# Optimization experiments

Measured on AMD Instinct MI355X. Metric: run time of the kernel, lower is better.

The kernel has to match this reference:

```python
import jax, jax.numpy as jnp
import numpy as np

NUM_USERS = 1024
NUM_BUSINESSES = 2048
N_NODES = NUM_USERS + NUM_BUSINESSES  # 3072
B = 1024            # batch size (== NUM_USERS to keep the business_idx-offset bug valid)
E = 16384           # edges (self loops added inside reference, PyG GATConv default)
H = 768             # hidden_size
HEADS = 8
NUM_IMAGES = 3


def setup_inputs() -> dict:
    key = jax.random.key(0)
    ks = jax.random.split(key, 24)
    def rn(k, shape, s=0.02):
        return jax.random.normal(k, shape, dtype=jnp.float32) * s
    inp = {
        'text_cls': rn(ks[0], (B, 768), 1.0),              # BERT CLS features
        'img_cls': rn(ks[1], (B, NUM_IMAGES, 768), 1.0),   # ViT CLS features per image
        'biz_feats': rn(ks[2], (B, 3), 1.0),
        'W_text': rn(ks[3], (768, H)), 'b_text': jnp.zeros((H,), jnp.float32),
        'W_img': rn(ks[4], (768, H)), 'b_img': jnp.zeros((H,), jnp.float32),
        'W_bf': rn(ks[5], (3, H)), 'b_bf': jnp.zeros((H,), jnp.float32),
        'user_table': rn(ks[6], (NUM_USERS, H)),
        'biz_table': rn(ks[7], (NUM_BUSINESSES, H)),
        'W1': rn(ks[8], (H, HEADS * H)),
        'att_src1': rn(ks[9], (HEADS, H), 0.1),
        'att_dst1': rn(ks[10], (HEADS, H), 0.1),
        'b1': jnp.zeros((HEADS * H,), jnp.float32),
        'W2': rn(ks[11], (HEADS * H, H)),
        'att_src2': rn(ks[12], (1, H), 0.1),
        'att_dst2': rn(ks[13], (1, H), 0.1),
        'b2': jnp.zeros((H,), jnp.float32),
        'Wf1': rn(ks[14], (4 * H, 2 * H)), 'bf1': jnp.zeros((2 * H,), jnp.float32),
        'Wf2': rn(ks[15], (2 * H, H)), 'bf2': jnp.zeros((H,), jnp.float32),
        'Wf3': rn(ks[16], (H, 1)), 'bf3': jnp.zeros((1,), jnp.float32),
        'user_idx': jax.random.randint(ks[17], (B,), 0, NUM_USERS),
        'business_idx': jax.random.randint(ks[18], (B,), NUM_USERS, N_NODES),
        'edge_index': jax.random.randint(ks[19], (2, E), 0, N_NODES),
    }
    return inp


def gat_conv(x, src, dst, W, a_src, a_dst, bias, heads):
    # PyG GATConv: linear -> per-head additive attention -> scatter softmax over dst -> scatter add
    N = x.shape[0]
    C = W.shape[1] // heads
    h = (x @ W).reshape(N, heads, C)                       # [N,H,C]
    s_src = jnp.sum(h * a_src, axis=-1)                    # [N,H]
    s_dst = jnp.sum(h * a_dst, axis=-1)                    # [N,H]
    e = jax.nn.leaky_relu(s_src[src] + s_dst[dst], 0.2)    # [E,H]
    e_max = jax.ops.segment_max(e, dst, num_segments=N)    # [N,H]
    ee = jnp.exp(e - e_max[dst])
    denom = jax.ops.segment_sum(ee, dst, num_segments=N)   # [N,H]
    alpha = ee / (denom[dst] + 1e-16)                      # [E,H]
    out = jax.ops.segment_sum(h[src] * alpha[..., None], dst, num_segments=N)  # [N,H,C]
    return out.reshape(N, heads * C) + bias


def reference(text_cls, img_cls, biz_feats, W_text, b_text, W_img, b_img, W_bf, b_bf,
              user_table, biz_table, W1, att_src1, att_dst1, b1, W2, att_src2, att_dst2, b2,
              Wf1, bf1, Wf2, bf2, Wf3, bf3, user_idx, business_idx, edge_index):
    text_emb = text_cls @ W_text + b_text                       # TextEncoder.fc
    img_emb = jnp.mean(img_cls, axis=1) @ W_img + b_img         # ImageEncoder mean + fc
    meta = biz_feats @ W_bf + b_bf                              # business_feature_fc
    user_emb = user_table[user_idx]
    biz_emb = biz_table[business_idx - user_idx.shape[0]]       # faithful: offset by batch size
    x = jnp.zeros((N_NODES, H), jnp.float32)
    x = x.at[user_idx].set(user_emb)
    x = x.at[business_idx].set((text_emb + img_emb + meta + biz_emb) / 4.0)
    loop = jnp.arange(N_NODES)
    src = jnp.concatenate([edge_index[0], loop])                # add self loops (PyG default)
    dst = jnp.concatenate([edge_index[1], loop])
    x = jax.nn.relu(gat_conv(x, src, dst, W1, att_src1, att_dst1, b1, HEADS))
    x = gat_conv(x, src, dst, W2, att_src2, att_dst2, b2, 1)
    cat = jnp.concatenate([x[user_idx], x[business_idx], text_emb, img_emb], axis=1)  # [B,4H]
    h1 = jax.nn.relu(cat @ Wf1 + bf1)
    h2 = jax.nn.relu(h1 @ Wf2 + bf2)
    return (h2 @ Wf3 + bf3).squeeze(-1)                         # [B]
```

## Files before the change

kernel.cpp:

```cpp
#include <hip/hip_runtime.h>
#include <hip/hip_bf16.h>

namespace {

constexpr int kB = 1024;
constexpr int kNU = 1024;
constexpr int kNB = 2048;
constexpr int kNN = 3072;
constexpr int kE = 16384;
constexpr int kET = kE + kNN;
constexpr int kH = 768;
constexpr int kHeads = 8;
constexpr int kS2 = 8;

typedef __attribute__((ext_vector_type(8))) short bf16x8_t;
typedef __attribute__((ext_vector_type(4))) float f32x4_t;

__device__ __forceinline__ float tof(float x) { return x; }
__device__ __forceinline__ float tof(__hip_bfloat16 x) { return __bfloat162float(x); }
__device__ __forceinline__ void stor(float* p, float v) { *p = v; }
__device__ __forceinline__ void stor(__hip_bfloat16* p, float v) { *p = __float2bfloat16(v); }

__device__ __forceinline__ float blo(unsigned u) {
  union { unsigned u; float f; } c; c.u = u << 16; return c.f;
}
__device__ __forceinline__ float bhi(unsigned u) {
  union { unsigned u; float f; } c; c.u = u & 0xffff0000u; return c.f;
}

__device__ __forceinline__ unsigned pk2(float a, float b) {
  union { __hip_bfloat16 h[2]; unsigned u; } c;
  c.h[0] = __float2bfloat16(a); c.h[1] = __float2bfloat16(b);
  return c.u;
}

__device__ __forceinline__ void gload_lds16(const void* g, void* l) {
  __builtin_amdgcn_global_load_lds(
      (const __attribute__((address_space(1))) void*)g,
      (__attribute__((address_space(3))) void*)l, 16, 0, 0);
}

template <int BM, int BN, int FM, int FN, typename TC>
__device__ __forceinline__ void gemm_body(
    const __hip_bfloat16* __restrict__ A, const __hip_bfloat16* __restrict__ Bt,
    const float* __restrict__ bias, TC* __restrict__ C,
    int K, int lda, int ldc, int act, int bx, int by) {
  __shared__ __align__(16) __hip_bfloat16 As[2][BM][32];
  __shared__ __align__(16) __hip_bfloat16 Bs[2][BN][32];
  const int t = threadIdx.x;
  const int w = t >> 6, lane = t & 63;
  const int wm = w >> 1, wn = w & 1;
  const int bm = by * BM, bn = bx * BN;
  const int lr = lane & 15, lg = lane >> 4;

  f32x4_t acc[FM][FN];
#pragma unroll
  for (int m = 0; m < FM; ++m)
#pragma unroll
    for (int n = 0; n < FN; ++n) acc[m][n] = (f32x4_t){0.f, 0.f, 0.f, 0.f};

  auto stage = [&](int buf, int kt) {
    const int k0 = kt << 5;
#pragma unroll
    for (int i = 0; i < BM / 64; ++i) {
      int L = i * 256 + t;
      gload_lds16(A + (size_t)(bm + (L >> 2)) * lda + k0 + (L & 3) * 8,
                  (char*)(&As[buf][0][0]) + ((size_t)(i * 256 + w * 64)) * 16);
    }
#pragma unroll
    for (int i = 0; i < BN / 64; ++i) {
      int L = i * 256 + t;
      gload_lds16(Bt + (size_t)(bn + (L >> 2)) * K + k0 + (L & 3) * 8,
                  (char*)(&Bs[buf][0][0]) + ((size_t)(i * 256 + w * 64)) * 16);
    }
  };

  const int NT = K >> 5;
  stage(0, 0);
  __syncthreads();
  for (int kt = 0; kt < NT; ++kt) {
    const int cur = kt & 1;
    if (kt + 1 < NT) stage(cur ^ 1, kt + 1);
    bf16x8_t af[FM], bv[FN];
#pragma unroll
    for (int m = 0; m < FM; ++m)
      af[m] = *(const bf16x8_t*)&As[cur][wm * FM * 16 + m * 16 + lr][lg * 8];
#pragma unroll
    for (int n = 0; n < FN; ++n)
      bv[n] = *(const bf16x8_t*)&Bs[cur][wn * FN * 16 + n * 16 + lr][lg * 8];
#pragma unroll
    for (int m = 0; m < FM; ++m)
#pragma unroll
      for (int n = 0; n < FN; ++n)
        acc[m][n] = __builtin_amdgcn_mfma_f32_16x16x32_bf16(af[m], bv[n], acc[m][n], 0, 0, 0);
    __syncthreads();
  }

#pragma unroll
  for (int m = 0; m < FM; ++m) {
    const int row0 = bm + wm * FM * 16 + m * 16 + lg * 4;
#pragma unroll
    for (int n = 0; n < FN; ++n) {
      const int cn = bn + wn * FN * 16 + n * 16 + lr;
      const float bvv = bias ? bias[cn] : 0.f;
#pragma unroll
      for (int r = 0; r < 4; ++r) {
        float v = acc[m][n][r] + bvv;
        if (act) v = fmaxf(v, 0.f);
        stor(&C[(size_t)(row0 + r) * ldc + cn], v);
      }
    }
  }
}

__device__ __forceinline__ void swz_xy(bool mfast, int& bx, int& by) {
  const int nwg = gridDim.x * gridDim.y;
  const int orig = blockIdx.y * gridDim.x + blockIdx.x;
  const int swz = (orig & 7) * (nwg >> 3) + (orig >> 3);
  if (mfast) { by = swz % gridDim.y; bx = swz / gridDim.y; }
  else       { bx = swz % gridDim.x; by = swz / gridDim.x; }
}

template <int BM, int BN, int FM, int FN>
__global__ __launch_bounds__(256) void mfma_gemm_dual(
    const __hip_bfloat16* __restrict__ A0, const __hip_bfloat16* __restrict__ Bt0,
    const float* __restrict__ bias0, float* __restrict__ C0,
    const __hip_bfloat16* __restrict__ A1, const __hip_bfloat16* __restrict__ Bt1,
    const float* __restrict__ bias1, float* __restrict__ C1,
    int N, int K) {
  int bx, by;
  swz_xy(true, bx, by);
  const __hip_bfloat16* A = blockIdx.z ? A1 : A0;
  const __hip_bfloat16* Bt = blockIdx.z ? Bt1 : Bt0;
  const float* bias = blockIdx.z ? bias1 : bias0;
  float* C = blockIdx.z ? C1 : C0;
  gemm_body<BM, BN, FM, FN, float>(A, Bt, bias, C, K, K, N, 0, bx, by);
}

template <int BM, int BN, int FM, int FN>
__global__ __launch_bounds__(256) void gemm_head(
    const __hip_bfloat16* __restrict__ y, const __hip_bfloat16* __restrict__ W1t,
    const float* __restrict__ b1, __hip_bfloat16* __restrict__ x2) {
  const int hd = blockIdx.x;
  const int tile = blockIdx.y;
  const int bx = tile % (kH / BN);
  const int by = tile / (kH / BN);
  gemm_body<BM, BN, FM, FN, __hip_bfloat16>(
      y + (size_t)hd * kH, W1t + (size_t)hd * kH * kH, b1 + hd * kH,
      x2 + (size_t)hd * kH, kH, kHeads * kH, kHeads * kH, 1, bx, by);
}

template <int BM, int BN, int FM, int FN, int S>
__global__ __launch_bounds__(256) void mfma_gemm_kpin(
    const __hip_bfloat16* __restrict__ A, const __hip_bfloat16* __restrict__ Bt,
    float* __restrict__ Cpart, int M, int N, int K) {
  __shared__ __align__(16) __hip_bfloat16 As[2][BM][32];
  __shared__ __align__(16) __hip_bfloat16 Bs[2][BN][32];
  const int kc = blockIdx.x;
  const int tile = blockIdx.y;
  const int tilesN = N / BN;
  const int bx = tile % tilesN;
  const int by = tile / tilesN;
  const int KC = K / S;
  const int kbeg = kc * KC;
  const int t = threadIdx.x;
  const int w = t >> 6, lane = t & 63;
  const int wm = w >> 1, wn = w & 1;
  const int bm = by * BM, bn = bx * BN;
  const int lr = lane & 15, lg = lane >> 4;

  f32x4_t acc[FM][FN];
#pragma unroll
  for (int m = 0; m < FM; ++m)
#pragma unroll
    for (int n = 0; n < FN; ++n) acc[m][n] = (f32x4_t){0.f, 0.f, 0.f, 0.f};

  auto stage = [&](int buf, int kt) {
    const int k0 = kbeg + (kt << 5);
#pragma unroll
    for (int i = 0; i < BM / 64; ++i) {
      int L = i * 256 + t;
      gload_lds16(A + (size_t)(bm + (L >> 2)) * K + k0 + (L & 3) * 8,
                  (char*)(&As[buf][0][0]) + ((size_t)(i * 256 + w * 64)) * 16);
    }
#pragma unroll
    for (int i = 0; i < BN / 64; ++i) {
      int L = i * 256 + t;
      gload_lds16(Bt + (size_t)(bn + (L >> 2)) * K + k0 + (L & 3) * 8,
                  (char*)(&Bs[buf][0][0]) + ((size_t)(i * 256 + w * 64)) * 16);
    }
  };

  const int NT = KC >> 5;
  stage(0, 0);
  __syncthreads();
  for (int kt = 0; kt < NT; ++kt) {
    const int cur = kt & 1;
    if (kt + 1 < NT) stage(cur ^ 1, kt + 1);
    bf16x8_t af[FM], bv[FN];
#pragma unroll
    for (int m = 0; m < FM; ++m)
      af[m] = *(const bf16x8_t*)&As[cur][wm * FM * 16 + m * 16 + lr][lg * 8];
#pragma unroll
    for (int n = 0; n < FN; ++n)
      bv[n] = *(const bf16x8_t*)&Bs[cur][wn * FN * 16 + n * 16 + lr][lg * 8];
#pragma unroll
    for (int m = 0; m < FM; ++m)
#pragma unroll
      for (int n = 0; n < FN; ++n)
        acc[m][n] = __builtin_amdgcn_mfma_f32_16x16x32_bf16(af[m], bv[n], acc[m][n], 0, 0, 0);
    __syncthreads();
  }

  float* Cp = Cpart + (size_t)kc * M * N;
#pragma unroll
  for (int m = 0; m < FM; ++m) {
    const int row0 = bm + wm * FM * 16 + m * 16 + lg * 4;
#pragma unroll
    for (int n = 0; n < FN; ++n) {
      const int cn = bn + wn * FN * 16 + n * 16 + lr;
#pragma unroll
      for (int r = 0; r < 4; ++r) Cp[(size_t)(row0 + r) * N + cn] = acc[m][n][r];
    }
  }
}

template <int BM, int BN, int FM, int FN>
__global__ __launch_bounds__(256) void mfma_gemm_splitk(
    const __hip_bfloat16* __restrict__ A, const __hip_bfloat16* __restrict__ Bt,
    float* __restrict__ Cpart, int M, int N, int K, int KC) {
  __shared__ __align__(16) __hip_bfloat16 As[2][BM][32];
  __shared__ __align__(16) __hip_bfloat16 Bs[2][BN][32];
  int bx, by;
  swz_xy(false, bx, by);
  const int t = threadIdx.x;
  const int w = t >> 6, lane = t & 63;
  const int wm = w >> 1, wn = w & 1;
  const int bm = by * BM, bn = bx * BN;
  const int kbeg = blockIdx.z * KC;
  const int lr = lane & 15, lg = lane >> 4;

  f32x4_t acc[FM][FN];
#pragma unroll
  for (int m = 0; m < FM; ++m)
#pragma unroll
    for (int n = 0; n < FN; ++n) acc[m][n] = (f32x4_t){0.f, 0.f, 0.f, 0.f};

  auto stage = [&](int buf, int kt) {
    const int k0 = kbeg + (kt << 5);
#pragma unroll
    for (int i = 0; i < BM / 64; ++i) {
      int L = i * 256 + t;
      gload_lds16(A + (size_t)(bm + (L >> 2)) * K + k0 + (L & 3) * 8,
                  (char*)(&As[buf][0][0]) + ((size_t)(i * 256 + w * 64)) * 16);
    }
#pragma unroll
    for (int i = 0; i < BN / 64; ++i) {
      int L = i * 256 + t;
      gload_lds16(Bt + (size_t)(bn + (L >> 2)) * K + k0 + (L & 3) * 8,
                  (char*)(&Bs[buf][0][0]) + ((size_t)(i * 256 + w * 64)) * 16);
    }
  };

  const int NT = KC >> 5;
  stage(0, 0);
  __syncthreads();
  for (int kt = 0; kt < NT; ++kt) {
    const int cur = kt & 1;
    if (kt + 1 < NT) stage(cur ^ 1, kt + 1);
    bf16x8_t af[FM], bv[FN];
#pragma unroll
    for (int m = 0; m < FM; ++m)
      af[m] = *(const bf16x8_t*)&As[cur][wm * FM * 16 + m * 16 + lr][lg * 8];
#pragma unroll
    for (int n = 0; n < FN; ++n)
      bv[n] = *(const bf16x8_t*)&Bs[cur][wn * FN * 16 + n * 16 + lr][lg * 8];
#pragma unroll
    for (int m = 0; m < FM; ++m)
#pragma unroll
      for (int n = 0; n < FN; ++n)
        acc[m][n] = __builtin_amdgcn_mfma_f32_16x16x32_bf16(af[m], bv[n], acc[m][n], 0, 0, 0);
    __syncthreads();
  }

  float* Cp = Cpart + (size_t)blockIdx.z * M * N;
#pragma unroll
  for (int m = 0; m < FM; ++m) {
    const int row0 = bm + wm * FM * 16 + m * 16 + lg * 4;
#pragma unroll
    for (int n = 0; n < FN; ++n) {
      const int cn = bn + wn * FN * 16 + n * 16 + lr;
#pragma unroll
      for (int r = 0; r < 4; ++r) Cp[(size_t)(row0 + r) * N + cn] = acc[m][n][r];
    }
  }
}

__global__ __launch_bounds__(192) void reduce_scores2_kernel(
    const float* __restrict__ part, const float* __restrict__ att_src,
    const float* __restrict__ att_dst, __hip_bfloat16* __restrict__ h2,
    float* __restrict__ s_src, float* __restrict__ s_dst) {
  __shared__ float redS[3], redD[3];
  const int row = blockIdx.x;
  const int t = threadIdx.x;
  const int c = t * 4;
  const float* p = part + (size_t)row * kH + c;
  float4 s = *(const float4*)p;
#pragma unroll
  for (int z = 1; z < kS2; ++z) {
    float4 qv = *(const float4*)(p + (size_t)z * kNN * kH);
    s.x += qv.x; s.y += qv.y; s.z += qv.z; s.w += qv.w;
  }
  __hip_bfloat16 b0 = __float2bfloat16(s.x), b1 = __float2bfloat16(s.y);
  __hip_bfloat16 b2 = __float2bfloat16(s.z), b3 = __float2bfloat16(s.w);
  __hip_bfloat16* o = h2 + (size_t)row * kH + c;
  o[0] = b0; o[1] = b1; o[2] = b2; o[3] = b3;
  float f0 = tof(b0), f1 = tof(b1), f2 = tof(b2), f3 = tof(b3);
  float ss = f0 * att_src[c] + f1 * att_src[c + 1] + f2 * att_src[c + 2] + f3 * att_src[c + 3];
  float sd = f0 * att_dst[c] + f1 * att_dst[c + 1] + f2 * att_dst[c + 2] + f3 * att_dst[c + 3];
#pragma unroll
  for (int off = 32; off; off >>= 1) { ss += __shfl_down(ss, off); sd += __shfl_down(sd, off); }
  if ((t & 63) == 0) { redS[t >> 6] = ss; redD[t >> 6] = sd; }
  __syncthreads();
  if (t == 0) {
    s_src[row] = redS[0] + redS[1] + redS[2];
    s_dst[row] = redD[0] + redD[1] + redD[2];
  }
}

__global__ void reduce_relu_kernel(const float* __restrict__ part,
                                   const float* __restrict__ bias,
                                   __hip_bfloat16* __restrict__ outb, int MN4, int N) {
  int i = blockIdx.x * 256 + threadIdx.x;
  if (i >= MN4) return;
  float4 s = ((const float4*)part)[i];
  float4 p = ((const float4*)part)[(size_t)MN4 + i];
  int c = (i * 4) % N;
  float v0 = fmaxf(s.x + p.x + bias[c], 0.f);
  float v1 = fmaxf(s.y + p.y + bias[c + 1], 0.f);
  float v2 = fmaxf(s.z + p.z + bias[c + 2], 0.f);
  float v3 = fmaxf(s.w + p.w + bias[c + 3], 0.f);
  uint2 o;
  o.x = pk2(v0, v1); o.y = pk2(v2, v3);
  *(uint2*)(outb + (size_t)i * 4) = o;
}

__global__ __launch_bounds__(192) void reduce_final_kernel(
    const float* __restrict__ part, const float* __restrict__ bias,
    const float* __restrict__ Wf3, const float* __restrict__ bf3,
    float* __restrict__ out) {
  __shared__ float red[3];
  const int row = blockIdx.x;
  const int t = threadIdx.x;
  const int c = t * 4;
  const float* p0 = part + (size_t)row * kH + c;
  const float* p1 = p0 + (size_t)kB * kH;
  float4 a = *(const float4*)p0;
  float4 b = *(const float4*)p1;
  float v0 = fmaxf(a.x + b.x + bias[c], 0.f);
  float v1 = fmaxf(a.y + b.y + bias[c + 1], 0.f);
  float v2 = fmaxf(a.z + b.z + bias[c + 2], 0.f);
  float v3 = fmaxf(a.w + b.w + bias[c + 3], 0.f);
  float s = v0 * Wf3[c] + v1 * Wf3[c + 1] + v2 * Wf3[c + 2] + v3 * Wf3[c + 3];
#pragma unroll
  for (int off = 32; off; off >>= 1) s += __shfl_down(s, off);
  if ((t & 63) == 0) red[t >> 6] = s;
  __syncthreads();
  if (t == 0) out[row] = red[0] + red[1] + red[2] + bf3[0];
}

struct TJobs {
  const float* in[6];
  __hip_bfloat16* out[6];
  int K[6];
  int N[6];
  int start[7];
};

__global__ __launch_bounds__(256) void transp_prep_kernel(
    TJobs j, const float* __restrict__ text_cls, const float* __restrict__ img_cls,
    __hip_bfloat16* __restrict__ text_bf, __hip_bfloat16* __restrict__ imgm_bf,
    int prep_blocks, const float* __restrict__ W1, const float* __restrict__ a_src,
    const float* __restrict__ a_dst, float* __restrict__ wa,
    int wa_blocks, uint4* __restrict__ xb4, int* __restrict__ deg,
    int* __restrict__ winner) {
  __shared__ float tl[32][33];
  const int bid = blockIdx.x;
  const int t = threadIdx.x;
  if (bid >= j.start[6] + prep_blocks + wa_blocks) {
    int i = (bid - j.start[6] - prep_blocks - wa_blocks) * 256 + t;
    if (i < kNN * kH * 2 / 16) xb4[i] = (uint4){0u, 0u, 0u, 0u};
    if (i < kNN) deg[i] = 0;
    if (i < kNB) winner[i] = -1;
    return;
  }
  if (bid >= j.start[6] + prep_blocks) {
    int gw = ((bid - j.start[6] - prep_blocks) * 256 + t) >> 6;
    int lane = t & 63;
    if (gw >= kHeads * kH) return;
    int i = gw >> 3, hd = gw & 7;
    const float* wrow = W1 + (size_t)i * (kHeads * kH) + hd * kH;
    const float* as = a_src + (size_t)hd * kH;
    const float* ad = a_dst + (size_t)hd * kH;
    float ss = 0.f, sd = 0.f;
    for (int c = lane; c < kH; c += 64) {
      float wv = wrow[c];
      ss = fmaf(wv, as[c], ss);
      sd = fmaf(wv, ad[c], sd);
    }
#pragma unroll
    for (int o = 32; o; o >>= 1) { ss += __shfl_down(ss, o); sd += __shfl_down(sd, o); }
    if (lane == 0) {
      wa[hd * kH + i] = ss;
      wa[kHeads * kH + hd * kH + i] = sd;
    }
    return;
  }
  if (bid >= j.start[6]) {
    int idx = (bid - j.start[6]) * 256 + t;
    if (idx < kB * kH) {
      text_bf[idx] = __float2bfloat16(text_cls[idx]);
      int b = idx / kH, c = idx - b * kH;
      const float* p = img_cls + (size_t)b * 3 * kH + c;
      imgm_bf[idx] = __float2bfloat16((p[0] + p[kH] + p[2 * kH]) * (1.f / 3.f));
    }
    return;
  }
  int idx = 0;
#pragma unroll
  for (int q = 1; q < 6; ++q)
    if (bid >= j.start[q]) idx = q;
  const int tile = bid - j.start[idx];
  const int N = j.N[idx], K = j.K[idx];
  const int tilesN = N >> 5;
  const int n0 = (tile % tilesN) << 5, k0 = (tile / tilesN) << 5;
  const float* in = j.in[idx];
  __hip_bfloat16* out = j.out[idx];
  const int r = t >> 3, c = (t & 7) * 4;
#pragma unroll
  for (int i = 0; i < 4; ++i) tl[r][c + i] = in[(size_t)(k0 + r) * N + n0 + c + i];
  __syncthreads();
  __hip_bfloat16* op = out + (size_t)(n0 + r) * K + k0 + c;
#pragma unroll
  for (int i = 0; i < 4; ++i) op[i] = __float2bfloat16(tl[c + i][r]);
}

__global__ __launch_bounds__(256) void s1_kernel(const __hip_bfloat16* __restrict__ xb,
                                                 const float* __restrict__ wa,
                                                 float* __restrict__ s1s,
                                                 float* __restrict__ s1d) {
  __shared__ unsigned xrow[kH / 2];
  const int n = blockIdx.x;
  const int t = threadIdx.x;
  const unsigned* xp = (const unsigned*)(xb + (size_t)n * kH);
  if (t < 128) { xrow[t] = xp[t]; xrow[t + 128] = xp[t + 128]; xrow[t + 256] = xp[t + 256]; }
  __syncthreads();
  const int w = t >> 6, lane = t & 63;
  const float* ws0 = wa + (size_t)w * kH;
  const float* wd0 = wa + (size_t)(kHeads + w) * kH;
  const float* ws1 = wa + (size_t)(w + 4) * kH;
  const float* wd1 = wa + (size_t)(kHeads + w + 4) * kH;
  float s0 = 0.f, d0 = 0.f, s1 = 0.f, d1 = 0.f;
  for (int u = lane; u < kH / 2; u += 64) {
    unsigned v = xrow[u];
    float f0 = blo(v), f1 = bhi(v);
    int c = u * 2;
    s0 = fmaf(f0, ws0[c], fmaf(f1, ws0[c + 1], s0));
    d0 = fmaf(f0, wd0[c], fmaf(f1, wd0[c + 1], d0));
    s1 = fmaf(f0, ws1[c], fmaf(f1, ws1[c + 1], s1));
    d1 = fmaf(f0, wd1[c], fmaf(f1, wd1[c + 1], d1));
  }
#pragma unroll
  for (int o = 32; o; o >>= 1) {
    s0 += __shfl_down(s0, o); d0 += __shfl_down(d0, o);
    s1 += __shfl_down(s1, o); d1 += __shfl_down(d1, o);
  }
  if (lane == 0) {
    s1s[n * 8 + w] = s0;     s1d[n * 8 + w] = d0;
    s1s[n * 8 + w + 4] = s1; s1d[n * 8 + w + 4] = d1;
  }
}

__global__ __launch_bounds__(256) void agg1x_kernel(
    const int* __restrict__ rowptr, const int* __restrict__ cols,
    const float* __restrict__ s1s, const float* __restrict__ s1d,
    const __hip_bfloat16* __restrict__ xb, __hip_bfloat16* __restrict__ y) {
  __shared__ float mh[8], rdh[8], sdl[8];
  __shared__ float alph[128][9];
  const int n = blockIdx.x;
  const int t = threadIdx.x, w = t >> 6, lane = t & 63;
  const int beg = rowptr[n], end = rowptr[n + 1];
  if (t < 8) sdl[t] = s1d[n * 8 + t];
  __syncthreads();
#pragma unroll
  for (int p = 0; p < 2; ++p) {
    const int h = w + p * 4;
    const float sd = sdl[h];
    float m = -3.402823466e38f;
    for (int i = beg + lane; i < end; i += 64) {
      float e = s1s[(size_t)cols[i] * 8 + h] + sd;
      e = (e > 0.f) ? e : 0.2f * e;
      m = fmaxf(m, e);
    }
#pragma unroll
    for (int o = 32; o; o >>= 1) m = fmaxf(m, __shfl_xor(m, o));
    float ds = 0.f;
    for (int i = beg + lane; i < end; i += 64) {
      float e = s1s[(size_t)cols[i] * 8 + h] + sd;
      e = (e > 0.f) ? e : 0.2f * e;
      ds += expf(e - m);
    }
#pragma unroll
    for (int o = 32; o; o >>= 1) ds += __shfl_xor(ds, o);
    if (lane == 0) { mh[h] = m; rdh[h] = 1.f / (ds + 1e-16f); }
  }
  __syncthreads();

  float acc[8][4];
#pragma unroll
  for (int h = 0; h < 8; ++h)
#pragma unroll
    for (int q = 0; q < 4; ++q) acc[h][q] = 0.f;
  const int c0 = t * 4;

  for (int chunk = beg; chunk < end; chunk += 128) {
    const int cnt = min(128, end - chunk);
#pragma unroll
    for (int p = 0; p < 2; ++p) {
      const int h = w + p * 4;
      const float sd = sdl[h], m = mh[h], rd = rdh[h];
      for (int i = lane; i < cnt; i += 64) {
        float e = s1s[(size_t)cols[chunk + i] * 8 + h] + sd;
        e = (e > 0.f) ? e : 0.2f * e;
        alph[i][h] = expf(e - m) * rd;
      }
    }
    __syncthreads();
    if (t < 192) {
      for (int i = 0; i < cnt; ++i) {
        int src = cols[chunk + i];
        uint2 v = *(const uint2*)(xb + (size_t)src * kH + c0);
        float f0 = blo(v.x), f1 = bhi(v.x), f2 = blo(v.y), f3 = bhi(v.y);
#pragma unroll
        for (int h = 0; h < 8; ++h) {
          float a = alph[i][h];
          acc[h][0] = fmaf(a, f0, acc[h][0]);
          acc[h][1] = fmaf(a, f1, acc[h][1]);
          acc[h][2] = fmaf(a, f2, acc[h][2]);
          acc[h][3] = fmaf(a, f3, acc[h][3]);
        }
      }
    }
    __syncthreads();
  }
  if (t < 192) {
#pragma unroll
    for (int h = 0; h < 8; ++h) {
      uint2 o;
      o.x = pk2(acc[h][0], acc[h][1]);
      o.y = pk2(acc[h][2], acc[h][3]);
      *(uint2*)(y + ((size_t)n * 8 + h) * kH + c0) = o;
    }
  }
}

__global__ void deg_winner_kernel(const int* __restrict__ ei, int* __restrict__ deg,
                                  const int* __restrict__ business_idx,
                                  int* __restrict__ winner) {
  int e = blockIdx.x * 256 + threadIdx.x;
  if (e < kET) {
    int dst = (e < kE) ? ei[kE + e] : (e - kE);
    atomicAdd(&deg[dst], 1);
  }
  if (e < kB) atomicMax(&winner[business_idx[e] - kNU], e);
}

__global__ __launch_bounds__(1024) void scan_kernel(const int* __restrict__ deg,
                                                    int* __restrict__ rowptr,
                                                    int* __restrict__ cursor) {
  __shared__ int sums[1024];
  int t = threadIdx.x;
  int v0 = deg[t * 3], v1 = deg[t * 3 + 1], v2 = deg[t * 3 + 2];
  int s = v0 + v1 + v2;
  sums[t] = s;
  __syncthreads();
  for (int o = 1; o < 1024; o <<= 1) {
    int xv = (t >= o) ? sums[t - o] : 0;
    __syncthreads();
    sums[t] += xv;
    __syncthreads();
  }
  int excl = sums[t] - s;
  rowptr[t * 3] = excl;          cursor[t * 3] = excl;
  rowptr[t * 3 + 1] = excl + v0; cursor[t * 3 + 1] = excl + v0;
  rowptr[t * 3 + 2] = excl + v0 + v1; cursor[t * 3 + 2] = excl + v0 + v1;
  if (t == 1023) rowptr[kNN] = excl + s;
}

__global__ void fill_kernel(const int* __restrict__ ei, int* __restrict__ cursor,
                            int* __restrict__ cols) {
  int e = blockIdx.x * 256 + threadIdx.x;
  if (e >= kET) return;
  int src, dst;
  if (e < kE) { src = ei[e]; dst = ei[kE + e]; } else { src = dst = e - kE; }
  int pos = atomicAdd(&cursor[dst], 1);
  cols[pos] = src;
}

__global__ void build_x_kernel(const int* __restrict__ user_idx,
                               const float* __restrict__ user_table,
                               const int* __restrict__ winner,
                               const float* __restrict__ text_emb,
                               const float* __restrict__ img_emb,
                               const float* __restrict__ biz_feats,
                               const float* __restrict__ W_bf,
                               const float* __restrict__ b_bf,
                               const float* __restrict__ biz_table,
                               __hip_bfloat16* __restrict__ xb) {
  int b = blockIdx.x;
  if (b < kNU) {
    int node = user_idx[b];
    for (int c = threadIdx.x; c < kH; c += blockDim.x)
      xb[(size_t)node * kH + c] = __float2bfloat16(user_table[(size_t)node * kH + c]);
  } else {
    int m = b - kNU;
    int w = winner[m];
    if (w < 0) return;
    int node = kNU + m;
    float f0 = biz_feats[w * 3], f1 = biz_feats[w * 3 + 1], f2 = biz_feats[w * 3 + 2];
    for (int c = threadIdx.x; c < kH; c += blockDim.x) {
      float meta = f0 * W_bf[c] + f1 * W_bf[kH + c] + f2 * W_bf[2 * kH + c] + b_bf[c];
      float v = (text_emb[(size_t)w * kH + c] + img_emb[(size_t)w * kH + c] + meta +
                 biz_table[(size_t)m * kH + c]) * 0.25f;
      xb[(size_t)node * kH + c] = __float2bfloat16(v);
    }
  }
}

__global__ __launch_bounds__(256) void gat_agg_kernel(
    const int* __restrict__ rowptr, const int* __restrict__ cols,
    const float* __restrict__ s_src, const float* __restrict__ s_dst,
    const __hip_bfloat16* __restrict__ h, const float* __restrict__ bias,
    float* __restrict__ out_f, int total) {
  const int pair = blockIdx.x * 4 + (threadIdx.x >> 6);
  if (pair >= total) return;
  const int lane = threadIdx.x & 63;
  const int n = pair;
  const int beg = rowptr[n], end = rowptr[n + 1];
  const float sdv = s_dst[pair];

  float m = -3.402823466e38f;
  for (int i = beg + lane; i < end; i += 64) {
    float e = s_src[cols[i]] + sdv;
    e = (e > 0.f) ? e : 0.2f * e;
    m = fmaxf(m, e);
  }
#pragma unroll
  for (int o = 32; o; o >>= 1) m = fmaxf(m, __shfl_xor(m, o));

  float dsum = 0.f;
  for (int i = beg + lane; i < end; i += 64) {
    float e = s_src[cols[i]] + sdv;
    e = (e > 0.f) ? e : 0.2f * e;
    dsum += expf(e - m);
  }
#pragma unroll
  for (int o = 32; o; o >>= 1) dsum += __shfl_xor(dsum, o);
  const float rdsum = 1.f / (dsum + 1e-16f);

  float a[12];
#pragma unroll
  for (int q = 0; q < 12; ++q) a[q] = 0.f;
  const size_t hoff = (size_t)lane * 4;
  for (int i = beg; i < end; ++i) {
    int src = cols[i];
    float e = s_src[src] + sdv;
    e = (e > 0.f) ? e : 0.2f * e;
    float wgt = expf(e - m) * rdsum;
    const __hip_bfloat16* hp = h + (size_t)src * kH + hoff;
#pragma unroll
    for (int j = 0; j < 3; ++j) {
      uint2 v = *(const uint2*)(hp + j * 256);
      a[j * 4 + 0] = fmaf(wgt, blo(v.x), a[j * 4 + 0]);
      a[j * 4 + 1] = fmaf(wgt, bhi(v.x), a[j * 4 + 1]);
      a[j * 4 + 2] = fmaf(wgt, blo(v.y), a[j * 4 + 2]);
      a[j * 4 + 3] = fmaf(wgt, bhi(v.y), a[j * 4 + 3]);
    }
  }
  const size_t ob = (size_t)n * kH + hoff;
#pragma unroll
  for (int j = 0; j < 3; ++j) {
#pragma unroll
    for (int q = 0; q < 4; ++q)
      out_f[ob + j * 256 + q] = a[j * 4 + q] + bias[hoff + j * 256 + q];
  }
}

__global__ void cat_kernel(const float* __restrict__ xf, const float* __restrict__ text_emb,
                           const float* __restrict__ img_emb, const int* __restrict__ user_idx,
                           const int* __restrict__ business_idx, __hip_bfloat16* __restrict__ cat) {
  int b = blockIdx.x;
  int u = user_idx[b], z = business_idx[b];
  __hip_bfloat16* crow = cat + (size_t)b * 4 * kH;
  for (int c = threadIdx.x; c < kH; c += blockDim.x) {
    crow[c] = __float2bfloat16(xf[(size_t)u * kH + c]);
    crow[kH + c] = __float2bfloat16(xf[(size_t)z * kH + c]);
    crow[2 * kH + c] = __float2bfloat16(text_emb[(size_t)b * kH + c]);
    crow[3 * kH + c] = __float2bfloat16(img_emb[(size_t)b * kH + c]);
  }
}

}

extern "C" void kernel_launch(void* const* d_in, const int* in_sizes, int n_in,
                              void* d_out, int out_size, void* d_ws, size_t ws_size,
                              hipStream_t stream) {
  const float* text_cls = (const float*)d_in[0];
  const float* img_cls = (const float*)d_in[1];
  const float* biz_feats = (const float*)d_in[2];
  const float* W_text = (const float*)d_in[3];
  const float* b_text = (const float*)d_in[4];
  const float* W_img = (const float*)d_in[5];
  const float* b_img = (const float*)d_in[6];
  const float* W_bf = (const float*)d_in[7];
  const float* b_bf = (const float*)d_in[8];
  const float* user_table = (const float*)d_in[9];
  const float* biz_table = (const float*)d_in[10];
  const float* W1 = (const float*)d_in[11];
  const float* att_src1 = (const float*)d_in[12];
  const float* att_dst1 = (const float*)d_in[13];
  const float* b1 = (const float*)d_in[14];
  const float* W2 = (const float*)d_in[15];
  const float* att_src2 = (const float*)d_in[16];
  const float* att_dst2 = (const float*)d_in[17];
  const float* b2 = (const float*)d_in[18];
  const float* Wf1 = (const float*)d_in[19];
  const float* bf1 = (const float*)d_in[20];
  const float* Wf2 = (const float*)d_in[21];
  const float* bf2 = (const float*)d_in[22];
  const float* Wf3 = (const float*)d_in[23];
  const float* bf3 = (const float*)d_in[24];
  const int* user_idx = (const int*)d_in[25];
  const int* business_idx = (const int*)d_in[26];
  const int* edge_index = (const int*)d_in[27];
  float* out = (float*)d_out;
  (void)in_sizes; (void)n_in; (void)out_size; (void)ws_size;

  char* base = (char*)d_ws;
  size_t off = 0;
  auto alloc = [&](size_t bytes) -> void* {
    void* p = base + off;
    off = (off + bytes + 255) & ~(size_t)255;
    return p;
  };
  __hip_bfloat16* xb = (__hip_bfloat16*)alloc((size_t)kNN * kH * 2);
  __hip_bfloat16* text_bf = (__hip_bfloat16*)alloc((size_t)kB * kH * 2);
  __hip_bfloat16* imgm_bf = (__hip_bfloat16*)alloc((size_t)kB * kH * 2);
  float* text_emb = (float*)alloc((size_t)kB * kH * 4);
  float* img_emb = (float*)alloc((size_t)kB * kH * 4);
  __hip_bfloat16* Wtt = (__hip_bfloat16*)alloc((size_t)kH * kH * 2);
  __hip_bfloat16* Wit = (__hip_bfloat16*)alloc((size_t)kH * kH * 2);
  __hip_bfloat16* W1t = (__hip_bfloat16*)alloc((size_t)kHeads * kH * kH * 2);
  __hip_bfloat16* W2t = (__hip_bfloat16*)alloc((size_t)kH * kHeads * kH * 2);
  __hip_bfloat16* Wf1t = (__hip_bfloat16*)alloc((size_t)2 * kH * 4 * kH * 2);
  __hip_bfloat16* Wf2t = (__hip_bfloat16*)alloc((size_t)kH * 2 * kH * 2);
  float* wa = (float*)alloc((size_t)2 * kHeads * kH * 4);
  __hip_bfloat16* y = (__hip_bfloat16*)alloc((size_t)kNN * kHeads * kH * 2);
  char* ext = (char*)alloc((size_t)kNN * kHeads * kH * 2);
  float* part = (float*)y;
  float* xf = (float*)ext;
  __hip_bfloat16* catb = (__hip_bfloat16*)(ext + 9437184);
  __hip_bfloat16* m1 = (__hip_bfloat16*)(ext + 9437184 + 6291456);
  __hip_bfloat16* x2 = (__hip_bfloat16*)alloc((size_t)kNN * kHeads * kH * 2);
  __hip_bfloat16* h2 = (__hip_bfloat16*)alloc((size_t)kNN * kH * 2);
  float* s1s = (float*)alloc((size_t)kNN * kHeads * 4);
  float* s1d = (float*)alloc((size_t)kNN * kHeads * 4);
  float* s2s = (float*)alloc((size_t)kNN * 4);
  float* s2d = (float*)alloc((size_t)kNN * 4);
  int* deg = (int*)alloc((size_t)kNN * 4);
  int* rowptr = (int*)alloc((size_t)(kNN + 1) * 4);
  int* cursor = (int*)alloc((size_t)kNN * 4);
  int* cols = (int*)alloc((size_t)kET * 4);
  int* winner = (int*)alloc((size_t)kNB * 4);

  TJobs tj;
  tj.in[0] = W_text; tj.out[0] = Wtt;  tj.K[0] = kH;          tj.N[0] = kH;
  tj.in[1] = W_img;  tj.out[1] = Wit;  tj.K[1] = kH;          tj.N[1] = kH;
  tj.in[2] = W1;     tj.out[2] = W1t;  tj.K[2] = kH;          tj.N[2] = kHeads * kH;
  tj.in[3] = W2;     tj.out[3] = W2t;  tj.K[3] = kHeads * kH; tj.N[3] = kH;
  tj.in[4] = Wf1;    tj.out[4] = Wf1t; tj.K[4] = 4 * kH;      tj.N[4] = 2 * kH;
  tj.in[5] = Wf2;    tj.out[5] = Wf2t; tj.K[5] = 2 * kH;      tj.N[5] = kH;
  tj.start[0] = 0;
  for (int q = 0; q < 6; ++q)
    tj.start[q + 1] = tj.start[q] + (tj.K[q] / 32) * (tj.N[q] / 32);
  const int prep_blocks = (kB * kH + 255) / 256;
  const int wa_blocks = (kHeads * kH) / 4;
  const int init_blocks = (kNN * kH * 2 / 16 + 255) / 256;
  transp_prep_kernel<<<tj.start[6] + prep_blocks + wa_blocks + init_blocks, 256, 0, stream>>>(
      tj, text_cls, img_cls, text_bf, imgm_bf, prep_blocks, W1, att_src1, att_dst1, wa,
      wa_blocks, (uint4*)xb, deg, winner);

  mfma_gemm_dual<64, 128, 2, 4><<<dim3(kH / 128, kB / 64, 2), 256, 0, stream>>>(
      text_bf, Wtt, b_text, text_emb, imgm_bf, Wit, b_img, img_emb, kH, kH);

  deg_winner_kernel<<<(kET + 255) / 256, 256, 0, stream>>>(edge_index, deg, business_idx, winner);
  scan_kernel<<<1, 1024, 0, stream>>>(deg, rowptr, cursor);
  fill_kernel<<<(kET + 255) / 256, 256, 0, stream>>>(edge_index, cursor, cols);

  build_x_kernel<<<kNN, 256, 0, stream>>>(user_idx, user_table, winner, text_emb, img_emb,
                                          biz_feats, W_bf, b_bf, biz_table, xb);

  s1_kernel<<<kNN, 256, 0, stream>>>(xb, wa, s1s, s1d);
  agg1x_kernel<<<kNN, 256, 0, stream>>>(rowptr, cols, s1s, s1d, xb, y);
  gemm_head<128, 128, 4, 4><<<dim3(kHeads, (kNN / 128) * (kH / 128)), 256, 0, stream>>>(
      y, W1t, b1, x2);

  mfma_gemm_kpin<128, 128, 4, 4, kS2>
      <<<dim3(kS2, (kNN / 128) * (kH / 128)), 256, 0, stream>>>(
          x2, W2t, part, kNN, kH, kHeads * kH);
  reduce_scores2_kernel<<<kNN, 192, 0, stream>>>(part, att_src2, att_dst2, h2, s2s, s2d);
  gat_agg_kernel<<<kNN / 4, 256, 0, stream>>>(rowptr, cols, s2s, s2d, h2, b2, xf, kNN);

  cat_kernel<<<kB, 256, 0, stream>>>(xf, text_emb, img_emb, user_idx, business_idx, catb);
  mfma_gemm_splitk<64, 128, 2, 4><<<dim3(2 * kH / 128, kB / 64, 2), 256, 0, stream>>>(
      catb, Wf1t, (float*)y, kB, 2 * kH, 4 * kH, 2 * kH);
  reduce_relu_kernel<<<(kB * 2 * kH / 4 + 255) / 256, 256, 0, stream>>>(
      (float*)y, bf1, m1, kB * 2 * kH / 4, 2 * kH);
  mfma_gemm_splitk<64, 128, 2, 4><<<dim3(kH / 128, kB / 64, 2), 256, 0, stream>>>(
      m1, Wf2t, (float*)y, kB, kH, 2 * kH, kH);
  reduce_final_kernel<<<kB, 192, 0, stream>>>((float*)y, bf2, Wf3, bf3, out);
}
```

Measured before the change: 263.6 us.

## Triple-buffer GEMM LDS pipeline and fuse graph-build kernels

All MFMA GEMM kernels move from double-buffered LDS staging with two __syncthreads per step to a three-stage ring. Each step waits with explicit vmcnt counts and a single s_barrier, prefetching two tiles ahead so global-to-LDS loads overlap more compute. Separately, degree counting moves into the scan kernel using shared-memory atomics, and the winner lookup is done inside a fused fill+build_x kernel, dropping two launches and the global deg/winner buffers. The ring raises LDS use per block, which may reduce occupancy, and the vmcnt counts assume exactly G loads per stage.

```diff
diff --git a/kernel.cpp b/kernel.cpp
--- a/kernel.cpp
+++ b/kernel.cpp
@@ -40,13 +40,28 @@
       (__attribute__((address_space(3))) void*)l, 16, 0, 0);
 }
 
+template <int G>
+__device__ __forceinline__ void wait_stage(bool more) {
+  if (more) {
+    if constexpr (G == 2) asm volatile("s_waitcnt vmcnt(2)" ::: "memory");
+    else if constexpr (G == 3) asm volatile("s_waitcnt vmcnt(3)" ::: "memory");
+    else asm volatile("s_waitcnt vmcnt(4)" ::: "memory");
+  } else {
+    asm volatile("s_waitcnt vmcnt(0)" ::: "memory");
+  }
+  __builtin_amdgcn_sched_barrier(0);
+  asm volatile("s_barrier" ::: "memory");
+  __builtin_amdgcn_sched_barrier(0);
+}
+
 template <int BM, int BN, int FM, int FN, typename TC>
 __device__ __forceinline__ void gemm_body(
     const __hip_bfloat16* __restrict__ A, const __hip_bfloat16* __restrict__ Bt,
     const float* __restrict__ bias, TC* __restrict__ C,
     int K, int lda, int ldc, int act, int bx, int by) {
-  __shared__ __align__(16) __hip_bfloat16 As[2][BM][32];
-  __shared__ __align__(16) __hip_bfloat16 Bs[2][BN][32];
+  __shared__ __align__(16) __hip_bfloat16 As[3][BM][32];
+  __shared__ __align__(16) __hip_bfloat16 Bs[3][BN][32];
+  constexpr int G = BM / 64 + BN / 64;
   const int t = threadIdx.x;
   const int w = t >> 6, lane = t & 63;
   const int wm = w >> 1, wn = w & 1;
@@ -77,10 +92,14 @@
 
   const int NT = K >> 5;
   stage(0, 0);
-  __syncthreads();
+  if (NT > 1) stage(1, 1);
+  int cur = 0;
   for (int kt = 0; kt < NT; ++kt) {
-    const int cur = kt & 1;
-    if (kt + 1 < NT) stage(cur ^ 1, kt + 1);
+    wait_stage<G>(kt + 1 < NT);
+    if (kt + 2 < NT) {
+      int sb = cur + 2; if (sb >= 3) sb -= 3;
+      stage(sb, kt + 2);
+    }
     bf16x8_t af[FM], bv[FN];
 #pragma unroll
     for (int m = 0; m < FM; ++m)
@@ -93,7 +112,7 @@
 #pragma unroll
       for (int n = 0; n < FN; ++n)
         acc[m][n] = __builtin_amdgcn_mfma_f32_16x16x32_bf16(af[m], bv[n], acc[m][n], 0, 0, 0);
-    __syncthreads();
+    cur = (cur == 2) ? 0 : cur + 1;
   }
 
 #pragma unroll
@@ -154,8 +173,9 @@
 __global__ __launch_bounds__(256) void mfma_gemm_kpin(
     const __hip_bfloat16* __restrict__ A, const __hip_bfloat16* __restrict__ Bt,
     float* __restrict__ Cpart, int M, int N, int K) {
-  __shared__ __align__(16) __hip_bfloat16 As[2][BM][32];
-  __shared__ __align__(16) __hip_bfloat16 Bs[2][BN][32];
+  __shared__ __align__(16) __hip_bfloat16 As[3][BM][32];
+  __shared__ __align__(16) __hip_bfloat16 Bs[3][BN][32];
+  constexpr int G = BM / 64 + BN / 64;
   const int kc = blockIdx.x;
   const int tile = blockIdx.y;
   const int tilesN = N / BN;
@@ -193,10 +213,14 @@
 
   const int NT = KC >> 5;
   stage(0, 0);
-  __syncthreads();
+  if (NT > 1) stage(1, 1);
+  int cur = 0;
   for (int kt = 0; kt < NT; ++kt) {
-    const int cur = kt & 1;
-    if (kt + 1 < NT) stage(cur ^ 1, kt + 1);
+    wait_stage<G>(kt + 1 < NT);
+    if (kt + 2 < NT) {
+      int sb = cur + 2; if (sb >= 3) sb -= 3;
+      stage(sb, kt + 2);
+    }
     bf16x8_t af[FM], bv[FN];
 #pragma unroll
     for (int m = 0; m < FM; ++m)
@@ -209,7 +233,7 @@
 #pragma unroll
       for (int n = 0; n < FN; ++n)
         acc[m][n] = __builtin_amdgcn_mfma_f32_16x16x32_bf16(af[m], bv[n], acc[m][n], 0, 0, 0);
-    __syncthreads();
+    cur = (cur == 2) ? 0 : cur + 1;
   }
 
   float* Cp = Cpart + (size_t)kc * M * N;
@@ -229,8 +253,9 @@
 __global__ __launch_bounds__(256) void mfma_gemm_splitk(
     const __hip_bfloat16* __restrict__ A, const __hip_bfloat16* __restrict__ Bt,
     float* __restrict__ Cpart, int M, int N, int K, int KC) {
-  __shared__ __align__(16) __hip_bfloat16 As[2][BM][32];
-  __shared__ __align__(16) __hip_bfloat16 Bs[2][BN][32];
+  __shared__ __align__(16) __hip_bfloat16 As[3][BM][32];
+  __shared__ __align__(16) __hip_bfloat16 Bs[3][BN][32];
+  constexpr int G = BM / 64 + BN / 64;
   int bx, by;
   swz_xy(false, bx, by);
   const int t = threadIdx.x;
@@ -264,10 +289,14 @@
 
   const int NT = KC >> 5;
   stage(0, 0);
-  __syncthreads();
+  if (NT > 1) stage(1, 1);
+  int cur = 0;
   for (int kt = 0; kt < NT; ++kt) {
-    const int cur = kt & 1;
-    if (kt + 1 < NT) stage(cur ^ 1, kt + 1);
+    wait_stage<G>(kt + 1 < NT);
+    if (kt + 2 < NT) {
+      int sb = cur + 2; if (sb >= 3) sb -= 3;
+      stage(sb, kt + 2);
+    }
     bf16x8_t af[FM], bv[FN];
 #pragma unroll
     for (int m = 0; m < FM; ++m)
@@ -280,7 +309,7 @@
 #pragma unroll
       for (int n = 0; n < FN; ++n)
         acc[m][n] = __builtin_amdgcn_mfma_f32_16x16x32_bf16(af[m], bv[n], acc[m][n], 0, 0, 0);
-    __syncthreads();
+    cur = (cur == 2) ? 0 : cur + 1;
   }
 
   float* Cp = Cpart + (size_t)blockIdx.z * M * N;
@@ -382,16 +411,13 @@
     __hip_bfloat16* __restrict__ text_bf, __hip_bfloat16* __restrict__ imgm_bf,
     int prep_blocks, const float* __restrict__ W1, const float* __restrict__ a_src,
     const float* __restrict__ a_dst, float* __restrict__ wa,
-    int wa_blocks, uint4* __restrict__ xb4, int* __restrict__ deg,
-    int* __restrict__ winner) {
+    int wa_blocks, uint4* __restrict__ xb4) {
   __shared__ float tl[32][33];
   const int bid = blockIdx.x;
   const int t = threadIdx.x;
   if (bid >= j.start[6] + prep_blocks + wa_blocks) {
     int i = (bid - j.start[6] - prep_blocks - wa_blocks) * 256 + t;
     if (i < kNN * kH * 2 / 16) xb4[i] = (uint4){0u, 0u, 0u, 0u};
-    if (i < kNN) deg[i] = 0;
-    if (i < kNB) winner[i] = -1;
     return;
   }
   if (bid >= j.start[6] + prep_blocks) {
@@ -564,23 +590,21 @@
   }
 }
 
-__global__ void deg_winner_kernel(const int* __restrict__ ei, int* __restrict__ deg,
-                                  const int* __restrict__ business_idx,
-                                  int* __restrict__ winner) {
-  int e = blockIdx.x * 256 + threadIdx.x;
-  if (e < kET) {
-    int dst = (e < kE) ? ei[kE + e] : (e - kE);
-    atomicAdd(&deg[dst], 1);
-  }
-  if (e < kB) atomicMax(&winner[business_idx[e] - kNU], e);
-}
-
-__global__ __launch_bounds__(1024) void scan_kernel(const int* __restrict__ deg,
+__global__ __launch_bounds__(1024) void scan_kernel(const int* __restrict__ ei,
                                                     int* __restrict__ rowptr,
                                                     int* __restrict__ cursor) {
+  __shared__ int sdeg[kNN];
   __shared__ int sums[1024];
   int t = threadIdx.x;
-  int v0 = deg[t * 3], v1 = deg[t * 3 + 1], v2 = deg[t * 3 + 2];
+#pragma unroll
+  for (int i = 0; i < 3; ++i) sdeg[t * 3 + i] = 0;
+  __syncthreads();
+  for (int e = t; e < kET; e += 1024) {
+    int dst = (e < kE) ? ei[kE + e] : (e - kE);
+    atomicAdd(&sdeg[dst], 1);
+  }
+  __syncthreads();
+  int v0 = sdeg[t * 3], v1 = sdeg[t * 3 + 1], v2 = sdeg[t * 3 + 2];
   int s = v0 + v1 + v2;
   sums[t] = s;
   __syncthreads();
@@ -597,38 +621,45 @@
   if (t == 1023) rowptr[kNN] = excl + s;
 }
 
-__global__ void fill_kernel(const int* __restrict__ ei, int* __restrict__ cursor,
-                            int* __restrict__ cols) {
-  int e = blockIdx.x * 256 + threadIdx.x;
-  if (e >= kET) return;
-  int src, dst;
-  if (e < kE) { src = ei[e]; dst = ei[kE + e]; } else { src = dst = e - kE; }
-  int pos = atomicAdd(&cursor[dst], 1);
-  cols[pos] = src;
-}
-
-__global__ void build_x_kernel(const int* __restrict__ user_idx,
-                               const float* __restrict__ user_table,
-                               const int* __restrict__ winner,
-                               const float* __restrict__ text_emb,
-                               const float* __restrict__ img_emb,
-                               const float* __restrict__ biz_feats,
-                               const float* __restrict__ W_bf,
-                               const float* __restrict__ b_bf,
-                               const float* __restrict__ biz_table,
-                               __hip_bfloat16* __restrict__ xb) {
-  int b = blockIdx.x;
+constexpr int kFillBlocks = (kET + 255) / 256;
+
+__global__ __launch_bounds__(256) void fill_build_kernel(
+    const int* __restrict__ ei, int* __restrict__ cursor, int* __restrict__ cols,
+    const int* __restrict__ user_idx, const float* __restrict__ user_table,
+    const int* __restrict__ business_idx, const float* __restrict__ text_emb,
+    const float* __restrict__ img_emb, const float* __restrict__ biz_feats,
+    const float* __restrict__ W_bf, const float* __restrict__ b_bf,
+    const float* __restrict__ biz_table, __hip_bfloat16* __restrict__ xb) {
+  const int bid = blockIdx.x;
+  if (bid < kFillBlocks) {
+    int e = bid * 256 + threadIdx.x;
+    if (e >= kET) return;
+    int src, dst;
+    if (e < kE) { src = ei[e]; dst = ei[kE + e]; } else { src = dst = e - kE; }
+    int pos = atomicAdd(&cursor[dst], 1);
+    cols[pos] = src;
+    return;
+  }
+  const int b = bid - kFillBlocks;
   if (b < kNU) {
     int node = user_idx[b];
-    for (int c = threadIdx.x; c < kH; c += blockDim.x)
+    for (int c = threadIdx.x; c < kH; c += 256)
       xb[(size_t)node * kH + c] = __float2bfloat16(user_table[(size_t)node * kH + c]);
   } else {
-    int m = b - kNU;
-    int w = winner[m];
+    const int m = b - kNU;
+    int cand = -1;
+    for (int i = threadIdx.x; i < kB; i += 256)
+      if (business_idx[i] == kNU + m) cand = i;
+#pragma unroll
+    for (int o = 32; o; o >>= 1) cand = max(cand, __shfl_xor(cand, o));
+    __shared__ int red[4];
+    if ((threadIdx.x & 63) == 0) red[threadIdx.x >> 6] = cand;
+    __syncthreads();
+    const int w = max(max(red[0], red[1]), max(red[2], red[3]));
     if (w < 0) return;
     int node = kNU + m;
     float f0 = biz_feats[w * 3], f1 = biz_feats[w * 3 + 1], f2 = biz_feats[w * 3 + 2];
-    for (int c = threadIdx.x; c < kH; c += blockDim.x) {
+    for (int c = threadIdx.x; c < kH; c += 256) {
       float meta = f0 * W_bf[c] + f1 * W_bf[kH + c] + f2 * W_bf[2 * kH + c] + b_bf[c];
       float v = (text_emb[(size_t)w * kH + c] + img_emb[(size_t)w * kH + c] + meta +
                  biz_table[(size_t)m * kH + c]) * 0.25f;
@@ -777,11 +808,9 @@
   float* s1d = (float*)alloc((size_t)kNN * kHeads * 4);
   float* s2s = (float*)alloc((size_t)kNN * 4);
   float* s2d = (float*)alloc((size_t)kNN * 4);
-  int* deg = (int*)alloc((size_t)kNN * 4);
   int* rowptr = (int*)alloc((size_t)(kNN + 1) * 4);
   int* cursor = (int*)alloc((size_t)kNN * 4);
   int* cols = (int*)alloc((size_t)kET * 4);
-  int* winner = (int*)alloc((size_t)kNB * 4);
 
   TJobs tj;
   tj.in[0] = W_text; tj.out[0] = Wtt;  tj.K[0] = kH;          tj.N[0] = kH;
@@ -798,17 +827,15 @@
   const int init_blocks = (kNN * kH * 2 / 16 + 255) / 256;
   transp_prep_kernel<<<tj.start[6] + prep_blocks + wa_blocks + init_blocks, 256, 0, stream>>>(
       tj, text_cls, img_cls, text_bf, imgm_bf, prep_blocks, W1, att_src1, att_dst1, wa,
-      wa_blocks, (uint4*)xb, deg, winner);
+      wa_blocks, (uint4*)xb);
 
   mfma_gemm_dual<64, 128, 2, 4><<<dim3(kH / 128, kB / 64, 2), 256, 0, stream>>>(
       text_bf, Wtt, b_text, text_emb, imgm_bf, Wit, b_img, img_emb, kH, kH);
 
-  deg_winner_kernel<<<(kET + 255) / 256, 256, 0, stream>>>(edge_index, deg, business_idx, winner);
-  scan_kernel<<<1, 1024, 0, stream>>>(deg, rowptr, cursor);
-  fill_kernel<<<(kET + 255) / 256, 256, 0, stream>>>(edge_index, cursor, cols);
-
-  build_x_kernel<<<kNN, 256, 0, stream>>>(user_idx, user_table, winner, text_emb, img_emb,
-                                          biz_feats, W_bf, b_bf, biz_table, xb);
+  scan_kernel<<<1, 1024, 0, stream>>>(edge_index, rowptr, cursor);
+  fill_build_kernel<<<kFillBlocks + kNN, 256, 0, stream>>>(
+      edge_index, cursor, cols, user_idx, user_table, business_idx, text_emb, img_emb,
+      biz_feats, W_bf, b_bf, biz_table, xb);
 
   s1_kernel<<<kNN, 256, 0, stream>>>(xb, wa, s1s, s1d);
   agg1x_kernel<<<kNN, 256, 0, stream>>>(rowptr, cols, s1s, s1d, xb, y);
```

Result: slower. 280.7 us (+6.5%).
